# Kernel tuning notes

Hardware: AMD Instinct MI355X
Metric: run time of the kernel (lower is better)

Reference implementation:

```python
import jax, jax.numpy as jnp
import numpy as np

N_IMG, N_TXT, D, H = 8192, 8192, 1024, 1024

def setup_inputs() -> dict:
    key = jax.random.key(0)
    ks = jax.random.split(key, 5)
    s = 0.02
    return {
        "img_feat": jax.random.normal(ks[0], (N_IMG, D), dtype=jnp.float32),
        "text_feat": jax.random.normal(ks[1], (N_TXT, D), dtype=jnp.float32),
        # nn.Linear weights stored as [out_features, in_features], applied as x @ W.T
        "W_Q": jax.random.normal(ks[2], (H, D), dtype=jnp.float32) * s,
        "W_K": jax.random.normal(ks[3], (H, D), dtype=jnp.float32) * s,
        "W_V": jax.random.normal(ks[4], (D, D), dtype=jnp.float32) * s,
    }

def reference(img_feat, text_feat, W_Q, W_K, W_V):
    scale = jnp.asarray(H, jnp.float32) ** -0.5
    Q = img_feat @ W_Q.T          # [N_img, H]
    K = text_feat @ W_K.T         # [N_txt, H]
    V = text_feat @ W_V.T         # [N_txt, D]
    attn_scores = (Q @ K.T) * scale          # [N_img, N_txt]
    attn_weights = jax.nn.softmax(attn_scores, axis=-1)
    cross_feat = attn_weights @ V             # [N_img, D]
    return cross_feat
```

## Files before the change

kernel.cpp:

```cpp
#include <hip/hip_runtime.h>
#include <hip/hip_bf16.h>

#define NI 8192
#define NT 8192
#define DD 1024
#define HH 1024

using bf16x8 = __attribute__((ext_vector_type(8))) __bf16;
using bf16x4 = __attribute__((ext_vector_type(4))) __bf16;
using f32x4  = __attribute__((ext_vector_type(4))) float;
using i32x4  = __attribute__((ext_vector_type(4))) int;

#define P_SCALE 12.0f

struct CvtArgs {
    const float* src[5];
    __bf16*      dst[5];
    int          blk_end[5];
};

__global__ void cvt_all_kernel(CvtArgs a) {
    int bid = blockIdx.x;
    int r = 0;
    while (bid >= a.blk_end[r]) ++r;
    int rbid = bid - (r ? a.blk_end[r - 1] : 0);
    int i = (rbid * 256 + threadIdx.x) * 4;
    float4 v = *(const float4*)(a.src[r] + i);
    bf16x4 o;
    o[0] = (__bf16)v.x; o[1] = (__bf16)v.y; o[2] = (__bf16)v.z; o[3] = (__bf16)v.w;
    *(bf16x4*)(a.dst[r] + i) = o;
}

__device__ __forceinline__ void async_copy16(const void* g, void* l) {
    __builtin_amdgcn_global_load_lds(
        (const __attribute__((address_space(1))) void*)g,
        (__attribute__((address_space(3))) void*)l,
        16, 0, 0);
}

__device__ __forceinline__ void gemm_tile_bf16(const __bf16* __restrict__ A,
                                               const __bf16* __restrict__ B,
                                               __bf16* As, __bf16* Bs,
                                               int bm, int bn, int lda, int ldb,
                                               int k0, int k1, f32x4 acc[4][4])
{
    const int t    = threadIdx.x;
    const int lane = t & 63;
    const int wave = t >> 6;
    const int wm   = wave >> 1;
    const int wn   = wave & 1;
    const int q    = lane >> 4;
    const int ml   = lane & 15;
    const int sw   = ml & 7;

    for (int kk = k0; kk < k1; kk += 64) {
#pragma unroll
        for (int it = 0; it < 4; ++it) {
            int idx = it * 256 + t;
            int r   = idx >> 3;
            int c   = ((idx & 7) ^ (r & 7)) << 3;
            async_copy16(A + (size_t)(bm + r) * lda + kk + c, As + idx * 8);
        }
#pragma unroll
        for (int it = 0; it < 4; ++it) {
            int idx = it * 256 + t;
            int r   = idx >> 3;
            int c   = ((idx & 7) ^ (r & 7)) << 3;
            async_copy16(B + (size_t)(bn + r) * ldb + kk + c, Bs + idx * 8);
        }
        __syncthreads();

#pragma unroll
        for (int ks = 0; ks < 64; ks += 32) {
            const int gb = ks >> 3;
            bf16x8 af[4], bfv[4];
#pragma unroll
            for (int rf = 0; rf < 4; ++rf)
                af[rf] = *(const bf16x8*)(As + (wm * 64 + rf * 16 + ml) * 64 +
                                          (((gb + q) ^ sw) << 3));
#pragma unroll
            for (int cf = 0; cf < 4; ++cf)
                bfv[cf] = *(const bf16x8*)(Bs + (wn * 64 + cf * 16 + ml) * 64 +
                                           (((gb + q) ^ sw) << 3));
#pragma unroll
            for (int rf = 0; rf < 4; ++rf)
#pragma unroll
                for (int cf = 0; cf < 4; ++cf)
                    acc[rf][cf] = __builtin_amdgcn_mfma_f32_16x16x32_bf16(
                        af[rf], bfv[cf], acc[rf][cf], 0, 0, 0);
        }
        __syncthreads();
    }
}

#define ACC_ZERO4(acc, T)                                    \
    _Pragma("unroll") for (int _i = 0; _i < 4; ++_i)         \
    _Pragma("unroll") for (int _j = 0; _j < 4; ++_j)         \
        acc[_i][_j] = (T){0, 0, 0, 0};


__device__ __forceinline__ void stage256(const char* __restrict__ g, char* l,
                                         int brow, int ld, int kk)
{
    const int t = threadIdx.x;
#pragma unroll
    for (int it = 0; it < 4; ++it) {
        int idx = it * 512 + t;
        int r   = idx >> 3;
        int c   = ((idx & 7) ^ (r & 7)) << 4;
        async_copy16(g + (size_t)(brow + r) * ld + kk + c, l + idx * 16);
    }
}

__device__ __forceinline__ void gemm256_i8(const char* __restrict__ A,
                                           const char* __restrict__ B,
                                           char (*As)[256 * 128],
                                           char (*Bs)[256 * 128],
                                           int bm, int bn, int lda, int ldb,
                                           int k0, int ntiles, i32x4 acc[8][4])
{
    const int lane = threadIdx.x & 63;
    const int wave = threadIdx.x >> 6;
    const int wm   = wave >> 2;
    const int wn   = wave & 3;
    const int q    = lane >> 4;
    const int ml   = lane & 15;
    const int sw   = ml & 7;

    stage256(A, As[0], bm, lda, k0);
    stage256(B, Bs[0], bn, ldb, k0);
    if (ntiles > 1) {
        stage256(A, As[1], bm, lda, k0 + 128);
        stage256(B, Bs[1], bn, ldb, k0 + 128);
        asm volatile("s_waitcnt vmcnt(8)" ::: "memory");
    } else {
        asm volatile("s_waitcnt vmcnt(0)" ::: "memory");
    }
    __builtin_amdgcn_s_barrier();

    for (int t = 0; t < ntiles; ++t) {
        const char* as = As[t & 1];
        const char* bs = Bs[t & 1];

        i32x4 bf[4][2];
#pragma unroll
        for (int n = 0; n < 4; ++n)
#pragma unroll
            for (int kh = 0; kh < 2; ++kh)
                bf[n][kh] = *(const i32x4*)(bs + (wn * 64 + n * 16 + ml) * 128 +
                                            (((kh * 4 + q) ^ sw) << 4));

#pragma unroll
        for (int ph = 0; ph < 4; ++ph) {
            i32x4 af[2][2];
#pragma unroll
            for (int m2 = 0; m2 < 2; ++m2)
#pragma unroll
                for (int kh = 0; kh < 2; ++kh)
                    af[m2][kh] = *(const i32x4*)(as +
                        (wm * 128 + (ph * 2 + m2) * 16 + ml) * 128 +
                        (((kh * 4 + q) ^ sw) << 4));
            __builtin_amdgcn_s_barrier();
            __builtin_amdgcn_s_setprio(1);
#pragma unroll
            for (int kh = 0; kh < 2; ++kh)
#pragma unroll
                for (int m2 = 0; m2 < 2; ++m2)
#pragma unroll
                    for (int n = 0; n < 4; ++n)
                        acc[ph * 2 + m2][n] = __builtin_amdgcn_mfma_i32_16x16x64_i8(
                            af[m2][kh], bf[n][kh], acc[ph * 2 + m2][n], 0, 0, 0);
            __builtin_amdgcn_s_setprio(0);
            __builtin_amdgcn_s_barrier();
        }
        __builtin_amdgcn_sched_barrier(0);
        if (t + 2 < ntiles) {
            stage256(A, As[t & 1], bm, lda, k0 + (t + 2) * 128);
            stage256(B, Bs[t & 1], bn, ldb, k0 + (t + 2) * 128);
            asm volatile("s_waitcnt vmcnt(8)" ::: "memory");
        } else {
            asm volatile("s_waitcnt vmcnt(0)" ::: "memory");
        }
        __builtin_amdgcn_s_barrier();
    }
}

__launch_bounds__(256, 4)
__global__ void qkv_kernel(const __bf16* __restrict__ imgb, const __bf16* __restrict__ textb,
                           const __bf16* __restrict__ wqb, const __bf16* __restrict__ wkb,
                           const __bf16* __restrict__ wvb,
                           __bf16* __restrict__ Qb, __bf16* __restrict__ Kb,
                           __bf16* __restrict__ Vtb)
{
    __shared__ __bf16 As[128 * 64];
    __shared__ __bf16 Bs[128 * 64];

    const int bid = blockIdx.x;
    const __bf16 *A, *B;
    __bf16* C;
    int N, bm, bn;
    if (bid < 512) {
        A = imgb;  B = wqb;   C = Qb;  N = 1024;
        bn = (bid & 7) * 128;  bm = (bid >> 3) * 128;
    } else if (bid < 1024) {
        A = textb; B = wkb;   C = Kb;  N = 1024;
        int r = bid - 512;  bn = (r & 7) * 128;  bm = (r >> 3) * 128;
    } else {
        A = wvb;   B = textb; C = Vtb; N = 8192;
        int r = bid - 1024; bn = (r & 63) * 128; bm = (r >> 6) * 128;
    }

    f32x4 acc[4][4];
    ACC_ZERO4(acc, f32x4);
    gemm_tile_bf16(A, B, As, Bs, bm, bn, DD, DD, 0, DD, acc);

    const int lane = threadIdx.x & 63, wave = threadIdx.x >> 6;
    const int wm = wave >> 1, wn = wave & 1, q = lane >> 4, ml = lane & 15;
#pragma unroll
    for (int rf = 0; rf < 4; ++rf)
#pragma unroll
        for (int i = 0; i < 4; ++i) {
            int row = bm + wm * 64 + rf * 16 + q * 4 + i;
#pragma unroll
            for (int cf = 0; cf < 4; ++cf) {
                int col = bn + wn * 64 + cf * 16 + ml;
                C[(size_t)row * N + col] = (__bf16)acc[rf][cf][i];
            }
        }
}

__device__ __forceinline__ float block_max(float m, float* red) {
#pragma unroll
    for (int o = 1; o < 64; o <<= 1) m = fmaxf(m, __shfl_xor(m, o));
    if ((threadIdx.x & 63) == 0) red[threadIdx.x >> 6] = m;
    __syncthreads();
    m = fmaxf(fmaxf(red[0], red[1]), fmaxf(red[2], red[3]));
    return m;
}

__global__ void quant_all_kernel(const __bf16* __restrict__ Qb, const __bf16* __restrict__ Kb,
                                 const __bf16* __restrict__ Vtb,
                                 char* __restrict__ Qq, char* __restrict__ Kq,
                                 char* __restrict__ Vtq,
                                 float* __restrict__ sQ, float* __restrict__ sK,
                                 float* __restrict__ sV, int* __restrict__ rsV,
                                 int* __restrict__ rdi)
{
    __shared__ float red[4];
    __shared__ int   redi[4];
    int bid = blockIdx.x;
    int t = threadIdx.x;

    if (bid < 2 * NI) {
        const __bf16* src; char* dst; float* sc; int r; bool isQ;
        if (bid < NI) { src = Qb; dst = Qq; sc = sQ; r = bid;      isQ = true;  }
        else          { src = Kb; dst = Kq; sc = sK; r = bid - NI; isQ = false; }
        src += (size_t)r * 1024;
        dst += (size_t)r * 1024;

        bf16x4 v = *(const bf16x4*)(src + t * 4);
        float x[4];
#pragma unroll
        for (int j = 0; j < 4; ++j) x[j] = (float)v[j];
        float m = fmaxf(fmaxf(fabsf(x[0]), fabsf(x[1])), fmaxf(fabsf(x[2]), fabsf(x[3])));
        m = fmaxf(block_max(m, red), 1e-20f);
        float qs = 127.0f / m;
        unsigned w = 0;
#pragma unroll
        for (int j = 0; j < 4; ++j) {
            int qv = (int)rintf(x[j] * qs);
            w |= ((unsigned)(qv & 0xff)) << (j * 8);
        }
        *(unsigned*)(dst + t * 4) = w;
        if (t == 0) {
            sc[r] = m / 127.0f;
            if (isQ) rdi[r] = 0;
        }
    } else {
        int row = bid - 2 * NI;
        const __bf16* src = Vtb + (size_t)row * NT;
        char* dst = Vtq + (size_t)row * NT;

        float m = 0.f;
#pragma unroll
        for (int c = 0; c < 4; ++c) {
            bf16x8 v = *(const bf16x8*)(src + t * 32 + c * 8);
#pragma unroll
            for (int j = 0; j < 8; ++j) m = fmaxf(m, fabsf((float)v[j]));
        }
        m = fmaxf(block_max(m, red), 1e-20f);
        float qs = 127.0f / m;

        int isum = 0;
        unsigned w[8];
#pragma unroll
        for (int k = 0; k < 8; ++k) {
            int dw = t * 8 + k;
            int b  = dw >> 4;
            int mm = dw & 15;
            unsigned ww = 0;
#pragma unroll
            for (int cf = 0; cf < 4; ++cf) {
                float x = (float)src[b * 64 + cf * 16 + mm];
                int qv = (int)rintf(x * qs);
                isum += qv;
                ww |= ((unsigned)(qv & 0xff)) << (cf * 8);
            }
            w[k] = ww;
        }
        *(uint4*)(dst + t * 32)      = make_uint4(w[0], w[1], w[2], w[3]);
        *(uint4*)(dst + t * 32 + 16) = make_uint4(w[4], w[5], w[6], w[7]);

#pragma unroll
        for (int o = 1; o < 64; o <<= 1) isum += __shfl_xor(isum, o);
        if ((t & 63) == 0) redi[t >> 6] = isum;
        __syncthreads();
        if (t == 0) {
            rsV[row]        = redi[0] + redi[1];
            rsV[1024 + row] = redi[2] + redi[3];
            sV[row] = m / 127.0f;
        }
    }
}

__launch_bounds__(512, 2)
__global__ void p_kernel_i8(const char* __restrict__ Qq, const char* __restrict__ Kq,
                            const float* __restrict__ sQ, const float* __restrict__ sK,
                            char* __restrict__ Pq, int* __restrict__ rdi)
{
    __shared__ char As[2][256 * 128];
    __shared__ char Bs[2][256 * 128];

    const int bn = blockIdx.x * 256;
    const int bm = blockIdx.y * 256;

    i32x4 acc[8][4];
#pragma unroll
    for (int i = 0; i < 8; ++i)
#pragma unroll
        for (int j = 0; j < 4; ++j) acc[i][j] = (i32x4){0, 0, 0, 0};

    gemm256_i8(Qq, Kq, As, Bs, bm, bn, 1024, 1024, 0, 8, acc);

    const int lane = threadIdx.x & 63, wave = threadIdx.x >> 6;
    const int wm = wave >> 2, wn = wave & 3, q = lane >> 4, ml = lane & 15;

#if __has_builtin(__builtin_amdgcn_exp2f)
    const float CADD = 4.40942084f;
    const float SMUL = 0.03125f * 1.44269504f;
#else
    const float CADD = 3.05635689f;
    const float SMUL = 0.03125f;
#endif

    float skc[4];
#pragma unroll
    for (int cf = 0; cf < 4; ++cf) skc[cf] = sK[bn + wn * 64 + cf * 16 + ml];

#pragma unroll
    for (int rf = 0; rf < 8; ++rf)
#pragma unroll
        for (int i = 0; i < 4; ++i) {
            int row = bm + wm * 128 + rf * 16 + q * 4 + i;
            float sr = sQ[row] * SMUL;
            unsigned w = 0;
            int usum = 0;
#pragma unroll
            for (int cf = 0; cf < 4; ++cf) {
                float tv  = (float)acc[rf][cf][i] * skc[cf];
                float arg = fmaf(tv, sr, CADD);
#if __has_builtin(__builtin_amdgcn_exp2f)
                float e = __builtin_amdgcn_exp2f(arg);
#else
                float e = __expf(arg);
#endif
                unsigned u = (unsigned)(e + 0.5f);
                usum += (int)u;
                w |= u << (cf * 8);
            }
            w ^= 0x80808080u;
            int isum = usum - 512;
            *(unsigned*)(Pq + (size_t)row * NT + bn + wn * 64 + 4 * ml) = w;
            isum += __shfl_xor(isum, 1);
            isum += __shfl_xor(isum, 2);
            isum += __shfl_xor(isum, 4);
            isum += __shfl_xor(isum, 8);
            if (ml == 0) atomicAdd(rdi + row, isum);
        }
}

__launch_bounds__(512, 2)
__global__ void o_kernel_i8(const char* __restrict__ Pq, const char* __restrict__ Vtq,
                            const int* __restrict__ rdi, const float* __restrict__ sV,
                            const int* __restrict__ rsV, float* __restrict__ out)
{
    __shared__ char As[2][256 * 128];
    __shared__ char Bs[2][256 * 128];

    const int bm = blockIdx.x * 256;
    const int bn = blockIdx.y * 256;
    const int k0 = blockIdx.z * (NT / 2);

    i32x4 acc[8][4];
#pragma unroll
    for (int i = 0; i < 8; ++i)
#pragma unroll
        for (int j = 0; j < 4; ++j) acc[i][j] = (i32x4){0, 0, 0, 0};

    gemm256_i8(Pq, Vtq, As, Bs, bm, bn, NT, NT, k0, (NT / 2) / 128, acc);

    const int lane = threadIdx.x & 63, wave = threadIdx.x >> 6;
    const int wm = wave >> 2, wn = wave & 3, q = lane >> 4, ml = lane & 15;

    float svc[4];
    int   rsc[4];
#pragma unroll
    for (int cf = 0; cf < 4; ++cf) {
        int col = bn + wn * 64 + cf * 16 + ml;
        svc[cf] = sV[col];
        rsc[cf] = rsV[blockIdx.z * 1024 + col];
    }

#pragma unroll
    for (int rf = 0; rf < 8; ++rf)
#pragma unroll
        for (int i = 0; i < 4; ++i) {
            int row = bm + wm * 128 + rf * 16 + q * 4 + i;
            float rd = 1.0f / (float)(rdi[row] + 128 * NT);
#pragma unroll
            for (int cf = 0; cf < 4; ++cf) {
                int col = bn + wn * 64 + cf * 16 + ml;
                float num = (float)(acc[rf][cf][i] + 128 * rsc[cf]);
                unsafeAtomicAdd(out + (size_t)row * DD + col, num * svc[cf] * rd);
            }
        }
}

extern "C" void kernel_launch(void* const* d_in, const int* in_sizes, int n_in,
                              void* d_out, int out_size, void* d_ws, size_t ws_size,
                              hipStream_t stream) {
    const float* img  = (const float*)d_in[0];
    const float* text = (const float*)d_in[1];
    const float* WQ   = (const float*)d_in[2];
    const float* WK   = (const float*)d_in[3];
    const float* WV   = (const float*)d_in[4];

    char* ws = (char*)d_ws;
    const size_t MB = 1024 * 1024;
    __bf16*  imgb  = (__bf16*)(ws);
    __bf16*  textb = (__bf16*)(ws + 16 * MB);
    __bf16*  wqb   = (__bf16*)(ws + 32 * MB);
    __bf16*  wkb   = (__bf16*)(ws + 34 * MB);
    __bf16*  wvb   = (__bf16*)(ws + 36 * MB);
    __bf16*  Qb    = (__bf16*)(ws + 38 * MB);
    __bf16*  Kb    = (__bf16*)(ws + 54 * MB);
    __bf16*  Vtb   = (__bf16*)(ws + 70 * MB);
    char*    Qq    = (char*)(ws + 86 * MB);
    char*    Kq    = (char*)(ws + 94 * MB);
    char*    Vtq   = (char*)(ws + 102 * MB);
    char*    Pq    = (char*)(ws + 110 * MB);
    float*   sQ    = (float*)(ws + 174 * MB);
    float*   sK    = (float*)(ws + 174 * MB + 32 * 1024);
    float*   sV    = (float*)(ws + 174 * MB + 64 * 1024);
    int*     rdi   = (int*)(ws + 174 * MB + 96 * 1024);
    int*     rsV   = (int*)(ws + 174 * MB + 128 * 1024);
    if (ws_size < 175 * MB) return;

    hipMemsetAsync(d_out, 0, (size_t)NI * DD * 4, stream);

    CvtArgs ca;
    ca.src[0] = img;  ca.dst[0] = imgb;
    ca.src[1] = text; ca.dst[1] = textb;
    ca.src[2] = WQ;   ca.dst[2] = wqb;
    ca.src[3] = WK;   ca.dst[3] = wkb;
    ca.src[4] = WV;   ca.dst[4] = wvb;
    int ends[5] = {NI * DD / 1024, NT * DD / 1024, HH * DD / 1024, HH * DD / 1024, DD * DD / 1024};
    int acc_e = 0;
    for (int i = 0; i < 5; ++i) { acc_e += ends[i]; ca.blk_end[i] = acc_e; }
    cvt_all_kernel<<<dim3(acc_e), dim3(256), 0, stream>>>(ca);

    qkv_kernel<<<dim3(1536), dim3(256), 0, stream>>>(imgb, textb, wqb, wkb, wvb,
                                                     Qb, Kb, Vtb);
    quant_all_kernel<<<dim3(2 * NI + DD), dim3(256), 0, stream>>>(
        Qb, Kb, Vtb, Qq, Kq, Vtq, sQ, sK, sV, rsV, rdi);
    p_kernel_i8<<<dim3(NT / 256, NI / 256), dim3(512), 0, stream>>>(Qq, Kq, sQ, sK,
                                                                    Pq, rdi);
    o_kernel_i8<<<dim3(NI / 256, DD / 256, 2), dim3(512), 0, stream>>>(Pq, Vtq,
                                                                       rdi, sV, rsV,
                                                                       (float*)d_out);
}
```

Baseline: 462.6 us.

## Interleave int8 GEMM tile loads across MFMA phases with split half-tile staging

Splits each 256-row tile copy into two 128-row halves and spreads the global-to-LDS async copies across the four MFMA phases of each k-tile, instead of issuing them all after the phase loop. A is now prefetched only one tile ahead, while B keeps a two-tile lead. B fragments are read at phase 0, and an explicit lgkmcnt wait plus sched_barrier is added before the MFMAs. The aim is to overlap memory traffic with matrix math and avoid a burst of copies between tiles. The shorter A prefetch distance and the added waits could expose latency.

```diff
diff --git a/kernel.cpp b/kernel.cpp
--- a/kernel.cpp
+++ b/kernel.cpp
@@ -99,12 +99,12 @@
         acc[_i][_j] = (T){0, 0, 0, 0};
 
 
-__device__ __forceinline__ void stage256(const char* __restrict__ g, char* l,
-                                         int brow, int ld, int kk)
+__device__ __forceinline__ void stage_half(const char* __restrict__ g, char* l,
+                                           int brow, int ld, int kk)
 {
     const int t = threadIdx.x;
 #pragma unroll
-    for (int it = 0; it < 4; ++it) {
+    for (int it = 0; it < 2; ++it) {
         int idx = it * 512 + t;
         int r   = idx >> 3;
         int c   = ((idx & 7) ^ (r & 7)) << 4;
@@ -127,11 +127,15 @@
     const int ml   = lane & 15;
     const int sw   = ml & 7;
 
-    stage256(A, As[0], bm, lda, k0);
-    stage256(B, Bs[0], bn, ldb, k0);
+    stage_half(A, As[0],         bm,       lda, k0);
+    stage_half(A, As[0] + 16384, bm + 128, lda, k0);
+    stage_half(B, Bs[0],         bn,       ldb, k0);
+    stage_half(B, Bs[0] + 16384, bn + 128, ldb, k0);
     if (ntiles > 1) {
-        stage256(A, As[1], bm, lda, k0 + 128);
-        stage256(B, Bs[1], bn, ldb, k0 + 128);
+        stage_half(A, As[1],         bm,       lda, k0 + 128);
+        stage_half(A, As[1] + 16384, bm + 128, lda, k0 + 128);
+        stage_half(B, Bs[1],         bn,       ldb, k0 + 128);
+        stage_half(B, Bs[1] + 16384, bn + 128, ldb, k0 + 128);
         asm volatile("s_waitcnt vmcnt(8)" ::: "memory");
     } else {
         asm volatile("s_waitcnt vmcnt(0)" ::: "memory");
@@ -141,17 +145,18 @@
     for (int t = 0; t < ntiles; ++t) {
         const char* as = As[t & 1];
         const char* bs = Bs[t & 1];
-
         i32x4 bf[4][2];
-#pragma unroll
-        for (int n = 0; n < 4; ++n)
-#pragma unroll
-            for (int kh = 0; kh < 2; ++kh)
-                bf[n][kh] = *(const i32x4*)(bs + (wn * 64 + n * 16 + ml) * 128 +
-                                            (((kh * 4 + q) ^ sw) << 4));
 
 #pragma unroll
         for (int ph = 0; ph < 4; ++ph) {
+            if (ph == 0) {
+#pragma unroll
+                for (int n = 0; n < 4; ++n)
+#pragma unroll
+                    for (int kh = 0; kh < 2; ++kh)
+                        bf[n][kh] = *(const i32x4*)(bs + (wn * 64 + n * 16 + ml) * 128 +
+                                                    (((kh * 4 + q) ^ sw) << 4));
+            }
             i32x4 af[2][2];
 #pragma unroll
             for (int m2 = 0; m2 < 2; ++m2)
@@ -160,7 +165,23 @@
                     af[m2][kh] = *(const i32x4*)(as +
                         (wm * 128 + (ph * 2 + m2) * 16 + ml) * 128 +
                         (((kh * 4 + q) ^ sw) << 4));
+
+            if (ph == 0) {
+                if (t >= 1 && t + 1 < ntiles) {
+                    stage_half(A, As[(t + 1) & 1],         bm,       lda, k0 + (t + 1) * 128);
+                    stage_half(A, As[(t + 1) & 1] + 16384, bm + 128, lda, k0 + (t + 1) * 128);
+                }
+            } else if (ph == 1) {
+                if (t + 2 < ntiles)
+                    stage_half(B, Bs[t & 1],         bn,       ldb, k0 + (t + 2) * 128);
+            } else if (ph == 2) {
+                if (t + 2 < ntiles)
+                    stage_half(B, Bs[t & 1] + 16384, bn + 128, ldb, k0 + (t + 2) * 128);
+            }
+
             __builtin_amdgcn_s_barrier();
+            asm volatile("s_waitcnt lgkmcnt(0)" ::: "memory");
+            __builtin_amdgcn_sched_barrier(0);
             __builtin_amdgcn_s_setprio(1);
 #pragma unroll
             for (int kh = 0; kh < 2; ++kh)
@@ -171,17 +192,14 @@
                         acc[ph * 2 + m2][n] = __builtin_amdgcn_mfma_i32_16x16x64_i8(
                             af[m2][kh], bf[n][kh], acc[ph * 2 + m2][n], 0, 0, 0);
             __builtin_amdgcn_s_setprio(0);
+            if (ph == 3 && t + 1 < ntiles) {
+                if (t + 2 < ntiles)
+                    asm volatile("s_waitcnt vmcnt(4)" ::: "memory");
+                else
+                    asm volatile("s_waitcnt vmcnt(0)" ::: "memory");
+            }
             __builtin_amdgcn_s_barrier();
         }
-        __builtin_amdgcn_sched_barrier(0);
-        if (t + 2 < ntiles) {
-            stage256(A, As[t & 1], bm, lda, k0 + (t + 2) * 128);
-            stage256(B, Bs[t & 1], bn, ldb, k0 + (t + 2) * 128);
-            asm volatile("s_waitcnt vmcnt(8)" ::: "memory");
-        } else {
-            asm volatile("s_waitcnt vmcnt(0)" ::: "memory");
-        }
-        __builtin_amdgcn_s_barrier();
     }
 }
 
```

New measurement: 448.7 us. -3.0%, faster.
